# Kernel tuning notes

Hardware: AMD Instinct MI355X
Metric: run time of the kernel (lower is better)

The kernel has to match this reference:

```python
import jax, jax.numpy as jnp
import numpy as np

NB_CODE_PER_HEAD = 512
NUM_HEADS = 2
NB_CODE = NB_CODE_PER_HEAD ** NUM_HEADS  # 262144
EPS = 1e-7


def setup_inputs() -> dict:
    key = jax.random.key(0)
    k1, k2 = jax.random.split(key)
    x = jax.random.normal(k1, (32, 512, 2048), dtype=jnp.float32)          # [N, code_dim, T]
    codebooks = jax.random.normal(k2, (NUM_HEADS, NB_CODE_PER_HEAD, 256),  # [H, K, d]
                                  dtype=jnp.float32)
    return {"x": x, "codebooks": codebooks}


def _nearest_codes(xt, codebooks):
    # xt: [N, T, H, d]; codebooks: [H, K, d] -> indices [N, T, H]
    # squared euclidean distance, argmin over K (the -2*x.c term is a GEMM)
    d2 = (jnp.sum(xt * xt, axis=-1, keepdims=True)
          - 2.0 * jnp.einsum('nthd,hkd->nthk', xt, codebooks)
          + jnp.sum(codebooks * codebooks, axis=-1)[None, None])  # [N, T, H, K]
    return jnp.argmin(d2, axis=-1)


def reference(x, codebooks):
    N, C, T = x.shape
    H, K, d = codebooks.shape
    xt = jnp.transpose(x, (0, 2, 1)).reshape(N, T, H, d)          # [N, T, H, d]
    idx = _nearest_codes(xt, codebooks)                           # [N, T, H]
    xq = codebooks[jnp.arange(H), idx]                            # gather -> [N, T, H, d]

    x_flat = xt.reshape(N, T, C)
    x_d = xq.reshape(N, T, C)

    # commit loss: F.mse_loss(x, x_d.detach())
    commit_loss = jnp.mean((x_flat - jax.lax.stop_gradient(x_d)) ** 2)

    # straight-through estimator
    x_ste = x_flat + jax.lax.stop_gradient(x_d - x_flat)
    out = jnp.transpose(x_ste, (0, 2, 1))                         # [N, C, T]

    # overall-index perplexity (from_mh_indices_to_overall_indices + histogram)
    powers = K ** jnp.arange(H, dtype=jnp.int32)                  # [1, K, K^2, ...]
    overall = jnp.sum(idx.astype(jnp.int32) * powers, axis=-1).reshape(-1)
    counts = jnp.bincount(overall, length=NB_CODE).astype(jnp.float32)
    prob = counts / jnp.sum(counts)
    perplexity = jnp.exp(-jnp.sum(prob * jnp.log(prob + EPS)))

    return out, commit_loss, perplexity
```

## Files before the change

### kernel.cpp

```cpp
#include <hip/hip_runtime.h>

#define N_ 32
#define C_ 512
#define T_ 2048
#define H_ 2
#define K_ 512
#define D_ 256
#define NBINS (K_ * K_)
#define TT 64
#define DELTA 0.6f

typedef __bf16 bf16x8 __attribute__((ext_vector_type(8)));
typedef float f32x4 __attribute__((ext_vector_type(4)));

__device__ __forceinline__ unsigned short f2b(float f) {
    return __builtin_bit_cast(unsigned short, (__bf16)f);
}
__device__ __forceinline__ float bf2f(unsigned bits_lo16) {
    return __builtin_bit_cast(float, bits_lo16 << 16);
}

__global__ void prep_k(const float* __restrict__ cb, float* __restrict__ cnorm,
                       float* __restrict__ cnb, unsigned short* __restrict__ cbb) {
    const int id = blockIdx.x;
    const int lane = threadIdx.x;
    const float4 v = *(const float4*)(cb + (size_t)id * D_ + lane * 4);
    __bf16 b0 = (__bf16)v.x, b1 = (__bf16)v.y, b2 = (__bf16)v.z, b3 = (__bf16)v.w;
    ushort4 uu;
    uu.x = __builtin_bit_cast(unsigned short, b0);
    uu.y = __builtin_bit_cast(unsigned short, b1);
    uu.z = __builtin_bit_cast(unsigned short, b2);
    uu.w = __builtin_bit_cast(unsigned short, b3);
    *(ushort4*)(cbb + (size_t)id * D_ + lane * 4) = uu;
    float f0 = (float)b0, f1 = (float)b1, f2 = (float)b2, f3 = (float)b3;
    float s32 = v.x * v.x + v.y * v.y + v.z * v.z + v.w * v.w;
    float sbb = f0 * f0 + f1 * f1 + f2 * f2 + f3 * f3;
    #pragma unroll
    for (int m = 1; m <= 32; m <<= 1) {
        s32 += __shfl_xor(s32, m, 64);
        sbb += __shfl_xor(sbb, m, 64);
    }
    if (lane == 0) { cnorm[id] = s32; cnb[id] = sbb; }
}

__global__ __launch_bounds__(256, 2) void vq_main(
    const float* __restrict__ x, const float* __restrict__ cbf,
    const float* __restrict__ cnorm, const float* __restrict__ cnb,
    const unsigned short* __restrict__ cbb,
    float* __restrict__ out, int* __restrict__ idx_ws, float* __restrict__ commit)
{
    __shared__ __align__(16) unsigned char SM[70736];
    unsigned short* xsb = (unsigned short*)SM;
    unsigned char*  cbs = SM + 32768;
    float* win   = (float*)(SM + 32768);
    float* xrw   = (float*)(SM + 66048);
    int*   idx_sh = (int*)(SM + 70144);
    float* wred  = (float*)(SM + 70400);
    int*   rl    = (int*)(SM + 70416);

    const int tid = threadIdx.x;
    const int lane = tid & 63;
    const int w = tid >> 6;
    const int n = blockIdx.y, h = blockIdx.z;
    const int t0 = blockIdx.x * TT;
    const size_t xbase = (size_t)n * C_ * T_ + (size_t)h * D_ * T_;

    const uint4* cbb4 = (const uint4*)(cbb + (size_t)(h * K_) * D_);
    uint4 creg[4];
    {
        const int sb0 = w * 4096 + lane * 16;
        #pragma unroll
        for (int it = 0; it < 4; ++it)
            creg[it] = cbb4[(sb0 + it * 1024) >> 4];
    }

    {
        const int tq = lane & 15, dl = lane >> 4;
        const float* xp = x + xbase + (size_t)(w * 64 + dl) * T_ + t0 + 4 * tq;
        const int t = 4 * tq + dl;
        #pragma unroll
        for (int i = 0; i < 16; ++i) {
            float4 v = *(const float4*)(xp + (size_t)(4 * i) * T_);
            float a0 = v.x, a1 = v.y, a2 = v.z, a3 = v.w;
            { float s = (lane & 16) ? a0 : a1; s = __shfl_xor(s, 16, 64); if (lane & 16) a0 = s; else a1 = s; }
            { float s = (lane & 16) ? a2 : a3; s = __shfl_xor(s, 16, 64); if (lane & 16) a2 = s; else a3 = s; }
            { float s = (lane & 32) ? a0 : a2; s = __shfl_xor(s, 32, 64); if (lane & 32) a0 = s; else a2 = s; }
            { float s = (lane & 32) ? a1 : a3; s = __shfl_xor(s, 32, 64); if (lane & 32) a1 = s; else a3 = s; }
            uint2 pk;
            pk.x = (unsigned)f2b(a0) | ((unsigned)f2b(a1) << 16);
            pk.y = (unsigned)f2b(a2) | ((unsigned)f2b(a3) << 16);
            const int off = (w * 64 + 4 * i) * 2;
            *(uint2*)((unsigned char*)xsb + t * 512 + (off ^ ((t & 7) << 4))) = pk;
        }
    }

    #pragma unroll
    for (int it = 0; it < 4; ++it) {
        const int sb = w * 4096 + it * 1024 + lane * 16;
        const int code = sb >> 9, off = sb & 511;
        *(uint4*)(cbs + code * 512 + (off ^ ((code & 7) << 4))) = creg[it];
    }
    __syncthreads();

    uint4 au[8];
    const int tA = 16 * w + (lane & 15);
    const int koff = (lane >> 4) * 16;
    #pragma unroll
    for (int kt = 0; kt < 8; ++kt) {
        const int off = kt * 64 + koff;
        au[kt] = *(const uint4*)((unsigned char*)xsb + tA * 512 + (off ^ ((tA & 7) << 4)));
    }

    float m1[4], m2[4]; int k1[4];
    #pragma unroll
    for (int q = 0; q < 4; ++q) { m1[q] = 3e38f; m2[q] = 3e38f; k1[q] = 0; }
    unsigned d2s[32][2];
    const int col = lane & 15;

    #pragma unroll
    for (int kc = 0; kc < 16; ++kc) {
        const int buf = (kc & 1) * 16384;
        if (kc < 15) {
            const int sb0 = w * 4096 + lane * 16;
            #pragma unroll
            for (int it = 0; it < 4; ++it)
                creg[it] = cbb4[((kc + 1) * 16384 + sb0 + it * 1024) >> 4];
        }
        const float cn0 = cnb[h * K_ + kc * 32 + col];
        const float cn1 = cnb[h * K_ + kc * 32 + 16 + col];

        #pragma unroll
        for (int sub = 0; sub < 2; ++sub) {
            const int c32 = sub * 16 + col;
            f32x4 acc = {0.f, 0.f, 0.f, 0.f};
            #pragma unroll
            for (int kt = 0; kt < 8; ++kt) {
                uint4 bu = *(const uint4*)(cbs + buf + c32 * 512 + ((kt * 64 + koff) ^ ((c32 & 7) << 4)));
                acc = __builtin_amdgcn_mfma_f32_16x16x32_bf16(
                        __builtin_bit_cast(bf16x8, au[kt]),
                        __builtin_bit_cast(bf16x8, bu), acc, 0, 0, 0);
            }
            const float cn = sub ? cn1 : cn0;
            const int code = kc * 32 + sub * 16 + col;
            float d2q[4];
            #pragma unroll
            for (int q = 0; q < 4; ++q) {
                const float d = fmaf(-2.f, acc[q], cn);
                d2q[q] = d;
                const float mx = fmaxf(d, m1[q]);
                m2[q] = fminf(m2[q], mx);
                const bool lt = d < m1[q];
                k1[q] = lt ? code : k1[q];
                m1[q] = lt ? d : m1[q];
            }
            d2s[kc * 2 + sub][0] = (unsigned)f2b(d2q[0]) | ((unsigned)f2b(d2q[1]) << 16);
            d2s[kc * 2 + sub][1] = (unsigned)f2b(d2q[2]) | ((unsigned)f2b(d2q[3]) << 16);
        }
        if (kc < 15) {
            #pragma unroll
            for (int it = 0; it < 4; ++it) {
                const int sb = w * 4096 + it * 1024 + lane * 16;
                const int code = sb >> 9, off = sb & 511;
                *(uint4*)(cbs + (buf ^ 16384) + code * 512 + (off ^ ((code & 7) << 4))) = creg[it];
            }
        }
        __syncthreads();
    }

    #pragma unroll
    for (int m = 1; m <= 8; m <<= 1) {
        #pragma unroll
        for (int q = 0; q < 4; ++q) {
            const float om1 = __shfl_xor(m1[q], m, 64);
            const int   ok  = __shfl_xor(k1[q], m, 64);
            const float om2 = __shfl_xor(m2[q], m, 64);
            const float nm2 = fminf(fminf(m2[q], om2), fmaxf(m1[q], om1));
            const bool sw = (om1 < m1[q]) || (om1 == m1[q] && ok < k1[q]);
            m1[q] = sw ? om1 : m1[q];
            k1[q] = sw ? ok : k1[q];
            m2[q] = nm2;
        }
    }

    if (lane == 0) rl[w * 20] = 0;
    const int g = lane >> 4;

    #pragma unroll
    for (int gg = 0; gg < 4; ++gg) {
        #pragma unroll
        for (int q = 0; q < 4; ++q) {
            const float bm1 = __shfl(m1[q], gg << 4, 64);
            const float bm2 = __shfl(m2[q], gg << 4, 64);
            if (bm2 < bm1 + DELTA) {
                const int row = 16 * w + 4 * gg + q;
                const float* xc = x + xbase + t0 + row;
                float4 xr;
                xr.x = xc[(size_t)(lane * 4 + 0) * T_];
                xr.y = xc[(size_t)(lane * 4 + 1) * T_];
                xr.z = xc[(size_t)(lane * 4 + 2) * T_];
                xr.w = xc[(size_t)(lane * 4 + 3) * T_];
                *(float4*)&xrw[w * 256 + lane * 4] = xr;
                if (g == gg) {
                    const float thrw = bm1 + (DELTA + 1.5f);
                    #pragma unroll
                    for (int i = 0; i < 32; ++i) {
                        const unsigned uu = d2s[i][q >> 1];
                        const float s = (q & 1) ? __builtin_bit_cast(float, uu & 0xffff0000u)
                                                : __builtin_bit_cast(float, uu << 16);
                        if (s < thrw) {
                            const int pos = atomicAdd(&rl[w * 20], 1);
                            if (pos < 19) rl[w * 20 + 1 + pos] = i * 16 + col;
                        }
                    }
                }
                __asm__ volatile("s_waitcnt lgkmcnt(0)" ::: "memory");
                int nc = rl[w * 20];
                if (nc > 19) nc = 19;
                float bv = 3e38f; int bk = 0x7fffffff;
                for (int ci = 0; ci < nc; ++ci) {
                    const int code = rl[w * 20 + 1 + ci];
                    const float4 xv = *(const float4*)&xrw[w * 256 + lane * 4];
                    const float4 cv = *(const float4*)&cbf[(size_t)(h * K_ + code) * D_ + lane * 4];
                    float d = xv.x * cv.x + xv.y * cv.y + xv.z * cv.z + xv.w * cv.w;
                    #pragma unroll
                    for (int mm = 1; mm <= 32; mm <<= 1) d += __shfl_xor(d, mm, 64);
                    const float d2x = cnorm[h * K_ + code] - 2.f * d;
                    if (d2x < bv || (d2x == bv && code < bk)) { bv = d2x; bk = code; }
                }
                if (g == gg) k1[q] = bk;
                if (lane == 0) rl[w * 20] = 0;
            }
        }
    }

    if ((lane & 15) == 0) {
        #pragma unroll
        for (int q = 0; q < 4; ++q) {
            const int row = 16 * w + 4 * g + q;
            idx_sh[row] = k1[q];
            idx_ws[((size_t)n * T_ + t0 + row) * H_ + h] = k1[q];
        }
    }
    __syncthreads();

    float csum = 0.f;
    #pragma unroll
    for (int ch = 0; ch < 2; ++ch) {
        #pragma unroll
        for (int rr = 0; rr < 8; ++rr) {
            const int row = ch * 32 + w * 8 + rr;
            const int code = idx_sh[row];
            const float4 cv = *(const float4*)&cbf[(size_t)(h * K_ + code) * D_ + lane * 4];
            const int off = (8 * lane) ^ ((row & 7) << 4);
            const uint2 pk = *(const uint2*)((unsigned char*)xsb + row * 512 + off);
            const float x0 = bf2f(pk.x & 0xffffu), x1 = bf2f(pk.x >> 16);
            const float x2 = bf2f(pk.y & 0xffffu), x3 = bf2f(pk.y >> 16);
            const float e0 = x0 - cv.x, e1 = x1 - cv.y, e2 = x2 - cv.z, e3 = x3 - cv.w;
            csum += e0 * e0 + e1 * e1 + e2 * e2 + e3 * e3;
            *(float4*)&win[(row & 31) * 260 + lane * 4] = cv;
        }
        __syncthreads();
        const int t32 = tid & 31, cg = tid >> 5;
        float* op = out + (size_t)n * C_ * T_ + (size_t)h * D_ * T_ + t0 + ch * 32 + t32;
        #pragma unroll
        for (int i = 0; i < 32; ++i) {
            const int c = cg + 8 * i;
            op[(size_t)c * T_] = win[t32 * 260 + c];
        }
        __syncthreads();
    }
    #pragma unroll
    for (int mm = 1; mm <= 32; mm <<= 1) csum += __shfl_xor(csum, mm, 64);
    if (lane == 0) wred[w] = csum;
    __syncthreads();
    if (tid == 0) atomicAdd(commit, wred[0] + wred[1] + wred[2] + wred[3]);
}

__global__ void hist_k(const int* __restrict__ idx_ws, int* __restrict__ counts) {
    const int gid = blockIdx.x * 256 + threadIdx.x;
    const int i0 = idx_ws[(size_t)gid * H_ + 0];
    const int i1 = idx_ws[(size_t)gid * H_ + 1];
    atomicAdd(&counts[i0 + K_ * i1], 1);
}

__global__ __launch_bounds__(256) void entropy_k(const int* __restrict__ counts,
                                                 float* __restrict__ ent) {
    __shared__ float red[4];
    const int tid = threadIdx.x;
    const int4 c4 = *(const int4*)(counts + 4 * (blockIdx.x * 256 + tid));
    float s = 0.f;
    {
        const float p0 = (float)c4.x * (1.f / 65536.f);
        const float p1 = (float)c4.y * (1.f / 65536.f);
        const float p2 = (float)c4.z * (1.f / 65536.f);
        const float p3 = (float)c4.w * (1.f / 65536.f);
        s = p0 * logf(p0 + 1e-7f) + p1 * logf(p1 + 1e-7f)
          + p2 * logf(p2 + 1e-7f) + p3 * logf(p3 + 1e-7f);
    }
    #pragma unroll
    for (int m = 1; m <= 32; m <<= 1) s += __shfl_xor(s, m, 64);
    if ((tid & 63) == 0) red[tid >> 6] = s;
    __syncthreads();
    if (tid == 0) atomicAdd(ent, red[0] + red[1] + red[2] + red[3]);
}

__global__ void final_k(const float* __restrict__ ent,
                        const float* __restrict__ commit,
                        float* __restrict__ outsc) {
    if (threadIdx.x == 0) {
        outsc[0] = commit[0] * (1.f / 33554432.f);
        outsc[1] = expf(-ent[0]);
    }
}

extern "C" void kernel_launch(void* const* d_in, const int* in_sizes, int n_in,
                              void* d_out, int out_size, void* d_ws, size_t ws_size,
                              hipStream_t stream) {
    const float* x  = (const float*)d_in[0];
    const float* cb = (const float*)d_in[1];
    float* out = (float*)d_out;

    char* ws = (char*)d_ws;
    int*   counts = (int*)ws;
    float* commit = (float*)(ws + 1048576);
    float* ent    = (float*)(ws + 1048580);
    float* cnorm  = (float*)(ws + 1048832);
    float* cnb    = (float*)(ws + 1052928);
    unsigned short* cbb = (unsigned short*)(ws + 1057024);
    int*   idx_ws = (int*)(ws + 1581312);

    hipMemsetAsync(d_ws, 0, 1048832, stream);
    prep_k<<<H_ * K_, 64, 0, stream>>>(cb, cnorm, cnb, cbb);
    vq_main<<<dim3(T_ / TT, N_, H_), 256, 0, stream>>>(x, cb, cnorm, cnb, cbb, out, idx_ws, commit);
    hist_k<<<N_ * T_ / 256, 256, 0, stream>>>(idx_ws, counts);
    entropy_k<<<NBINS / 1024, 256, 0, stream>>>(counts, ent);
    final_k<<<1, 64, 0, stream>>>(ent, commit, out + 33554432);
}
```

Before: 151.9 us.

## Alias x staging with codebook LDS to cut shared memory and raise occupancy

Cuts shared memory from about 70 KB to about 38 KB by reusing the x bf16 staging area for the codebook tiles. Each wave loads its A fragments into registers before the region is overwritten, which needs an extra barrier. Because the staged x is gone by the end, the commit-loss term is now computed from the register-held A fragments against the gathered codewords in the output window. Launch bounds go from 2 to 4 blocks per CU, raising occupancy at the cost of tighter register limits, which could cause spills.

```diff
diff --git a/kernel.cpp b/kernel.cpp
--- a/kernel.cpp
+++ b/kernel.cpp
@@ -43,20 +43,20 @@
     if (lane == 0) { cnorm[id] = s32; cnb[id] = sbb; }
 }
 
-__global__ __launch_bounds__(256, 2) void vq_main(
+__global__ __launch_bounds__(256, 4) void vq_main(
     const float* __restrict__ x, const float* __restrict__ cbf,
     const float* __restrict__ cnorm, const float* __restrict__ cnb,
     const unsigned short* __restrict__ cbb,
     float* __restrict__ out, int* __restrict__ idx_ws, float* __restrict__ commit)
 {
-    __shared__ __align__(16) unsigned char SM[70736];
-    unsigned short* xsb = (unsigned short*)SM;
-    unsigned char*  cbs = SM + 32768;
-    float* win   = (float*)(SM + 32768);
-    float* xrw   = (float*)(SM + 66048);
-    int*   idx_sh = (int*)(SM + 70144);
-    float* wred  = (float*)(SM + 70400);
-    int*   rl    = (int*)(SM + 70416);
+    __shared__ __align__(16) unsigned char SM[37968];
+    unsigned char*  xstage = SM;
+    unsigned char*  cbs    = SM;
+    float* win    = (float*)SM;
+    float* xrw    = (float*)(SM + 33280);
+    int*   idx_sh = (int*)(SM + 37376);
+    float* wred   = (float*)(SM + 37632);
+    int*   rl     = (int*)(SM + 37648);
 
     const int tid = threadIdx.x;
     const int lane = tid & 63;
@@ -90,9 +90,20 @@
             pk.x = (unsigned)f2b(a0) | ((unsigned)f2b(a1) << 16);
             pk.y = (unsigned)f2b(a2) | ((unsigned)f2b(a3) << 16);
             const int off = (w * 64 + 4 * i) * 2;
-            *(uint2*)((unsigned char*)xsb + t * 512 + (off ^ ((t & 7) << 4))) = pk;
-        }
-    }
+            *(uint2*)(xstage + t * 512 + (off ^ ((t & 7) << 4))) = pk;
+        }
+    }
+    __syncthreads();
+
+    uint4 au[8];
+    const int tA = 16 * w + (lane & 15);
+    const int koff = (lane >> 4) * 16;
+    #pragma unroll
+    for (int kt = 0; kt < 8; ++kt) {
+        const int off = kt * 64 + koff;
+        au[kt] = *(const uint4*)(xstage + tA * 512 + (off ^ ((tA & 7) << 4)));
+    }
+    __syncthreads();
 
     #pragma unroll
     for (int it = 0; it < 4; ++it) {
@@ -101,15 +112,6 @@
         *(uint4*)(cbs + code * 512 + (off ^ ((code & 7) << 4))) = creg[it];
     }
     __syncthreads();
-
-    uint4 au[8];
-    const int tA = 16 * w + (lane & 15);
-    const int koff = (lane >> 4) * 16;
-    #pragma unroll
-    for (int kt = 0; kt < 8; ++kt) {
-        const int off = kt * 64 + koff;
-        au[kt] = *(const uint4*)((unsigned char*)xsb + tA * 512 + (off ^ ((tA & 7) << 4)));
-    }
 
     float m1[4], m2[4]; int k1[4];
     #pragma unroll
@@ -251,15 +253,27 @@
             const int row = ch * 32 + w * 8 + rr;
             const int code = idx_sh[row];
             const float4 cv = *(const float4*)&cbf[(size_t)(h * K_ + code) * D_ + lane * 4];
-            const int off = (8 * lane) ^ ((row & 7) << 4);
-            const uint2 pk = *(const uint2*)((unsigned char*)xsb + row * 512 + off);
-            const float x0 = bf2f(pk.x & 0xffffu), x1 = bf2f(pk.x >> 16);
-            const float x2 = bf2f(pk.y & 0xffffu), x3 = bf2f(pk.y >> 16);
-            const float e0 = x0 - cv.x, e1 = x1 - cv.y, e2 = x2 - cv.z, e3 = x3 - cv.w;
-            csum += e0 * e0 + e1 * e1 + e2 * e2 + e3 * e3;
             *(float4*)&win[(row & 31) * 260 + lane * 4] = cv;
         }
         __syncthreads();
+        if ((w >> 1) == ch) {
+            const int r = tA & 31;
+            #pragma unroll
+            for (int kt = 0; kt < 8; ++kt) {
+                const float4 c0 = *(const float4*)&win[r * 260 + 32 * kt + 2 * koff];
+                const float4 c1 = *(const float4*)&win[r * 260 + 32 * kt + 2 * koff + 4];
+                const uint4 a = au[kt];
+                const float x0 = bf2f(a.x & 0xffffu), x1 = bf2f(a.x >> 16);
+                const float x2 = bf2f(a.y & 0xffffu), x3 = bf2f(a.y >> 16);
+                const float x4 = bf2f(a.z & 0xffffu), x5 = bf2f(a.z >> 16);
+                const float x6 = bf2f(a.w & 0xffffu), x7 = bf2f(a.w >> 16);
+                float e;
+                e = x0 - c0.x; csum += e * e;  e = x1 - c0.y; csum += e * e;
+                e = x2 - c0.z; csum += e * e;  e = x3 - c0.w; csum += e * e;
+                e = x4 - c1.x; csum += e * e;  e = x5 - c1.y; csum += e * e;
+                e = x6 - c1.z; csum += e * e;  e = x7 - c1.w; csum += e * e;
+            }
+        }
         const int t32 = tid & 31, cg = tid >> 5;
         float* op = out + (size_t)n * C_ * T_ + (size_t)h * D_ * T_ + t0 + ch * 32 + t32;
         #pragma unroll
```

Result: slower. 476.3 us (+213.5%).
